# Kernel optimization log

Hardware: AMD Instinct MI355X
Metric: run time of the kernel (lower is better)

## Reference

```python
import jax, jax.numpy as jnp
import numpy as np

WINDOW_SIZE = 512
NUM_HEADS = 16
HIDDEN = 1024
HEAD_DIM = HIDDEN // NUM_HEADS
SCALING = HEAD_DIM ** (-0.5)


def sliding_window_mask(seq_len, window_size):
    # row i attends to cols j with i - w//2 <= j <= i + w//2 (clipped to bounds)
    i = jnp.arange(seq_len)[:, None]
    j = jnp.arange(seq_len)[None, :]
    half = window_size // 2
    return jnp.abs(i - j) <= half  # [S, S] bool


def setup_inputs() -> dict:
    key = jax.random.key(0)
    k0, k1, k2, k3, k4 = jax.random.split(key, 5)
    B, S = 2, 2048
    hidden_states = jax.random.normal(k0, (B, S, HIDDEN), dtype=jnp.float32)
    scale = 0.02
    Wq = jax.random.normal(k1, (HIDDEN, HIDDEN), dtype=jnp.float32) * scale
    Wk = jax.random.normal(k2, (HIDDEN, HIDDEN), dtype=jnp.float32) * scale
    Wv = jax.random.normal(k3, (HIDDEN, HIDDEN), dtype=jnp.float32) * scale
    Wo = jax.random.normal(k4, (HIDDEN, HIDDEN), dtype=jnp.float32) * scale
    return {"hidden_states": hidden_states, "Wq": Wq, "Wk": Wk, "Wv": Wv, "Wo": Wo}


def reference(hidden_states, Wq, Wk, Wv, Wo):
    B, S, _ = hidden_states.shape
    # nn.Linear(bias=False): y = x @ W.T
    def proj(x, W):
        y = jnp.einsum('bsh,oh->bso', x, W)
        return y.reshape(B, S, NUM_HEADS, HEAD_DIM).transpose(0, 2, 1, 3)  # [B,H,S,D]

    q = proj(hidden_states, Wq)
    k = proj(hidden_states, Wk)
    v = proj(hidden_states, Wv)

    mask = sliding_window_mask(S, WINDOW_SIZE)  # [S,S]
    scores = jnp.einsum('bhsd,bhtd->bhst', q, k) * SCALING  # [B,H,S,S]
    scores = jnp.where(mask[None, None], scores, -jnp.inf)
    attn = jax.nn.softmax(scores, axis=-1)
    out = jnp.einsum('bhst,bhtd->bhsd', attn, v)
    out = out.transpose(0, 2, 1, 3).reshape(B, S, HIDDEN)
    out = jnp.einsum('bsh,oh->bso', out, Wo)
    return out, attn
```

## Files before the change

### kernel.cpp

```cpp
#include <hip/hip_runtime.h>

typedef unsigned short u16;
typedef __attribute__((ext_vector_type(8))) __bf16 bf16x8;
typedef __attribute__((ext_vector_type(4))) float f32x4;

#define DEV __device__ __forceinline__
#define SEQ 2048
#define SWZ(r) ((((r) & 7)) ^ (((r) >> 3) & 7))

DEV void async16(void* lds, const void* gptr) {
  __builtin_amdgcn_global_load_lds(
      (const __attribute__((address_space(1))) unsigned int*)gptr,
      (__attribute__((address_space(3))) unsigned int*)lds, 16, 0, 0);
}

DEV u16 f2bf(float x) {
  unsigned u = __float_as_uint(x);
  return (u16)((u + 0x7fffu + ((u >> 16) & 1u)) >> 16);
}

DEV f32x4 mfma(bf16x8 a, bf16x8 b, f32x4 c) {
  return __builtin_amdgcn_mfma_f32_16x16x32_bf16(a, b, c, 0, 0, 0);
}

__global__ __launch_bounds__(256) void k_cvt_all(
    const float* __restrict__ hs, const float* __restrict__ wq,
    const float* __restrict__ wk, const float* __restrict__ wv,
    const float* __restrict__ wo, u16* __restrict__ X16,
    u16* __restrict__ W16) {
  int b = blockIdx.x;
  const float* src;
  u16* dst;
  int off;
  if (b < 4096) {
    src = hs;
    dst = X16;
    off = b * 1024;
  } else {
    int b2 = b - 4096;
    int w = b2 >> 10;
    src = (w == 0) ? wq : (w == 1) ? wk : (w == 2) ? wv : wo;
    dst = W16 + (size_t)w * 1048576;
    off = (b2 & 1023) * 1024;
  }
  int i = off + threadIdx.x * 4;
  float4 v = *(const float4*)(src + i);
  *(ushort4*)(dst + i) = make_ushort4(f2bf(v.x), f2bf(v.y), f2bf(v.z), f2bf(v.w));
}

DEV void gemm_mainloop(const u16* __restrict__ A, const u16* __restrict__ B,
                       int K, u16* As, u16* Bs, f32x4 (&acc)[4][4], int tid) {
  const int wid = tid >> 6, lane = tid & 63;
  const int wm = wid >> 1, wn = wid & 1;
  const int quad = lane >> 4, l15 = lane & 15;
  const int ci0 = tid, ci1 = tid + 256;
  const int r0 = ci0 >> 2, g0 = (ci0 & 3) ^ (r0 & 3);
  const int r1 = ci1 >> 2, g1 = (ci1 & 3) ^ (r1 & 3);
  u16* ldsA0 = As + wid * 512;
  u16* ldsA1 = As + wid * 512 + 2048;
  u16* ldsB0 = Bs + wid * 512;
  u16* ldsB1 = Bs + wid * 512 + 2048;

  for (int k0 = 0; k0 < K; k0 += 32) {
    __syncthreads();
    async16(ldsA0, A + (size_t)r0 * K + k0 + g0 * 8);
    async16(ldsA1, A + (size_t)r1 * K + k0 + g1 * 8);
    async16(ldsB0, B + (size_t)r0 * K + k0 + g0 * 8);
    async16(ldsB1, B + (size_t)r1 * K + k0 + g1 * 8);
    __syncthreads();
    bf16x8 af[4], bf[4];
#pragma unroll
    for (int mt = 0; mt < 4; ++mt) {
      int row = wm * 64 + mt * 16 + l15;
      af[mt] = *(const bf16x8*)(As + row * 32 + (quad ^ (row & 3)) * 8);
    }
#pragma unroll
    for (int nt = 0; nt < 4; ++nt) {
      int row = wn * 64 + nt * 16 + l15;
      bf[nt] = *(const bf16x8*)(Bs + row * 32 + (quad ^ (row & 3)) * 8);
    }
#pragma unroll
    for (int mt = 0; mt < 4; ++mt)
#pragma unroll
      for (int nt = 0; nt < 4; ++nt)
        acc[mt][nt] = mfma(af[mt], bf[nt], acc[mt][nt]);
  }
}

__global__ __launch_bounds__(256) void k_gemm_qkv(
    const u16* __restrict__ X, const u16* __restrict__ Wq,
    const u16* __restrict__ Wk, const u16* __restrict__ Wv,
    u16* __restrict__ Q16, u16* __restrict__ K16, u16* __restrict__ V16) {
  __shared__ u16 As[128 * 32], Bs[128 * 32];
  const int tid = threadIdx.x;
  const int bm = blockIdx.x, bn = blockIdx.y, z = blockIdx.z;
  const u16* B = (z == 0) ? Wq : (z == 1) ? Wk : Wv;
  u16* dst = (z == 0) ? Q16 : (z == 1) ? K16 : V16;
  const float sc = (z == 0) ? 0.125f : 1.0f;
  f32x4 acc[4][4];
#pragma unroll
  for (int i = 0; i < 4; ++i)
#pragma unroll
    for (int j = 0; j < 4; ++j) acc[i][j] = (f32x4){0.f, 0.f, 0.f, 0.f};
  gemm_mainloop(X + (size_t)bm * 128 * 1024, B + (size_t)bn * 128 * 1024, 1024,
                As, Bs, acc, tid);
  const int wid = tid >> 6, lane = tid & 63;
  const int wm = wid >> 1, wn = wid & 1, quad = lane >> 4, l15 = lane & 15;
#pragma unroll
  for (int mt = 0; mt < 4; ++mt)
#pragma unroll
    for (int nt = 0; nt < 4; ++nt)
#pragma unroll
      for (int r = 0; r < 4; ++r) {
        int row = bm * 128 + wm * 64 + mt * 16 + quad * 4 + r;
        int col = bn * 128 + wn * 64 + nt * 16 + l15;
        int b = row >> 11, s = row & 2047, h = col >> 6, d = col & 63;
        int bh = b * 16 + h;
        dst[((size_t)bh * SEQ + s) * 64 + d] = f2bf(acc[mt][nt][r] * sc);
      }
}

__global__ __launch_bounds__(256) void k_gemm_out(const u16* __restrict__ A,
                                                  const u16* __restrict__ Bw,
                                                  float* __restrict__ out) {
  __shared__ u16 As[64 * 32], Bs[128 * 32];
  const int tid = threadIdx.x;
  const int wid = tid >> 6, lane = tid & 63;
  const int wm = wid >> 1, wn = wid & 1;
  const int quad = lane >> 4, l15 = lane & 15;
  const int rA = tid >> 2, gA = (tid & 3) ^ (rA & 3);
  const int r1 = (tid + 256) >> 2, g1 = ((tid + 256) & 3) ^ (r1 & 3);
  const u16* Ab = A + (size_t)blockIdx.x * 64 * 1024;
  const u16* Bb = Bw + (size_t)blockIdx.y * 128 * 1024;
  f32x4 acc[2][4];
#pragma unroll
  for (int i = 0; i < 2; ++i)
#pragma unroll
    for (int j = 0; j < 4; ++j) acc[i][j] = (f32x4){0.f, 0.f, 0.f, 0.f};

  for (int k0 = 0; k0 < 1024; k0 += 32) {
    __syncthreads();
    async16(As + wid * 512, Ab + (size_t)rA * 1024 + k0 + gA * 8);
    async16(Bs + wid * 512, Bb + (size_t)rA * 1024 + k0 + gA * 8);
    async16(Bs + wid * 512 + 2048, Bb + (size_t)r1 * 1024 + k0 + g1 * 8);
    __syncthreads();
    bf16x8 af[2], bf[4];
#pragma unroll
    for (int mt = 0; mt < 2; ++mt) {
      int row = wm * 32 + mt * 16 + l15;
      af[mt] = *(const bf16x8*)(As + row * 32 + (quad ^ (row & 3)) * 8);
    }
#pragma unroll
    for (int nt = 0; nt < 4; ++nt) {
      int row = wn * 64 + nt * 16 + l15;
      bf[nt] = *(const bf16x8*)(Bs + row * 32 + (quad ^ (row & 3)) * 8);
    }
#pragma unroll
    for (int mt = 0; mt < 2; ++mt)
#pragma unroll
      for (int nt = 0; nt < 4; ++nt)
        acc[mt][nt] = mfma(af[mt], bf[nt], acc[mt][nt]);
  }
#pragma unroll
  for (int mt = 0; mt < 2; ++mt)
#pragma unroll
    for (int nt = 0; nt < 4; ++nt)
#pragma unroll
      for (int r = 0; r < 4; ++r) {
        int row = blockIdx.x * 64 + wm * 32 + mt * 16 + quad * 4 + r;
        int col = blockIdx.y * 128 + wn * 64 + nt * 16 + l15;
        out[(size_t)row * 1024 + col] = acc[mt][nt][r];
      }
}

__global__ __launch_bounds__(256, 2) void k_attn(
    const u16* __restrict__ Q16, const u16* __restrict__ K16,
    const u16* __restrict__ V16, float* __restrict__ attn_out,
    u16* __restrict__ O16) {
  __shared__ union alignas(16) U {
    struct {
      u16 Qt[4096];
      u16 Kt[3][4096];
      u16 Vt[3][4096];
      u16 P[2][64 * 72];
    } s;
    float Pf[2][64 * 68];
  } sm;
  __shared__ float rowsum[64];

  const int tid = threadIdx.x, wid = tid >> 6, lane = tid & 63;
  const int quad = lane >> 4, l15 = lane & 15;
  const int qbase = blockIdx.x * 64;
  const int bh = blockIdx.y;
  const int b = bh >> 4, h = bh & 15;
  const u16* Qb = Q16 + ((size_t)bh * SEQ + qbase) * 64;
  const u16* Kb = K16 + (size_t)bh * SEQ * 64;
  const u16* Vb = V16 + (size_t)bh * SEQ * 64;
  float* attn_b = attn_out + (size_t)bh * SEQ * SEQ;

  const int r0 = tid >> 3, g0 = (tid & 7) ^ SWZ(r0);
  const int r1 = r0 + 32, g1 = (tid & 7) ^ SWZ(r1);

  const int tlo = qbase >= 256 ? 0 : (256 - qbase) >> 6;
  const int thi_raw = (SEQ - 64 - qbase + 256) >> 6;
  const int thi = thi_raw > 8 ? 8 : thi_raw;

  auto stage = [&](int t) {
    int jb = qbase - 256 + t * 64;
    u16* Kd = sm.s.Kt[t % 3];
    u16* Vd = sm.s.Vt[t % 3];
    async16(Kd + wid * 512, Kb + (size_t)(jb + r0) * 64 + g0 * 8);
    async16(Kd + wid * 512 + 2048, Kb + (size_t)(jb + r1) * 64 + g1 * 8);
    async16(Vd + wid * 512, Vb + (size_t)(jb + r0) * 64 + g0 * 8);
    async16(Vd + wid * 512 + 2048, Vb + (size_t)(jb + r1) * 64 + g1 * 8);
  };

  async16(sm.s.Qt + wid * 512, Qb + r0 * 64 + g0 * 8);
  async16(sm.s.Qt + wid * 512 + 2048, Qb + (size_t)r1 * 64 + g1 * 8);
  stage(tlo);
  if (tlo + 1 <= thi) stage(tlo + 1);
  if (tid < 64) rowsum[tid] = 0.f;

  float racc[4][4];
  f32x4 oacc[4];
#pragma unroll
  for (int mt = 0; mt < 4; ++mt) {
    oacc[mt] = (f32x4){0.f, 0.f, 0.f, 0.f};
#pragma unroll
    for (int r = 0; r < 4; ++r) racc[mt][r] = 0.f;
  }
  unsigned stash[9][8];
  bf16x8 bv_prev[2];
  bf16x8 aq[4][2];
  bool aq_loaded = false;
  const int d = wid * 16 + l15;

#pragma unroll
  for (int t = 0; t < 9; ++t) {
    if (t < tlo || t > thi) continue;
    const int jbase = qbase - 256 + t * 64;
    if (t + 1 <= thi)
      asm volatile("s_waitcnt vmcnt(4) lgkmcnt(0)" ::: "memory");
    else
      asm volatile("s_waitcnt vmcnt(0) lgkmcnt(0)" ::: "memory");
    __builtin_amdgcn_s_barrier();
    if (t + 2 <= thi) stage(t + 2);
    if (!aq_loaded) {
      aq_loaded = true;
#pragma unroll
      for (int mt = 0; mt < 4; ++mt)
#pragma unroll
        for (int ks = 0; ks < 2; ++ks) {
          int row = mt * 16 + l15;
          aq[mt][ks] = *(const bf16x8*)(sm.s.Qt + row * 64 +
                                        (((ks * 4 + quad) ^ SWZ(row)) * 8));
        }
    }
    if (t > tlo) {
      const u16* Pp = sm.s.P[(t + 1) & 1];
#pragma unroll
      for (int mt = 0; mt < 4; ++mt) {
        int row = mt * 16 + l15;
        bf16x8 ap0 = *(const bf16x8*)(Pp + row * 72 + quad * 8);
        bf16x8 ap1 = *(const bf16x8*)(Pp + row * 72 + 32 + quad * 8);
        oacc[mt] = mfma(ap0, bv_prev[0], oacc[mt]);
        oacc[mt] = mfma(ap1, bv_prev[1], oacc[mt]);
      }
    }
    const u16* Kt = sm.s.Kt[t % 3];
    const u16* Vtp = sm.s.Vt[t % 3];
    bf16x8 bq[2];
#pragma unroll
    for (int ks = 0; ks < 2; ++ks) {
      int row = wid * 16 + l15;
      bq[ks] = *(const bf16x8*)(Kt + row * 64 + (((ks * 4 + quad) ^ SWZ(row)) * 8));
    }
#pragma unroll
    for (int ks = 0; ks < 2; ++ks)
#pragma unroll
      for (int jj = 0; jj < 8; ++jj) {
        int j = ks * 32 + quad * 8 + jj;
        int slot = (d >> 3) ^ SWZ(j);
        bv_prev[ks][jj] = *(const __bf16*)(Vtp + j * 64 + slot * 8 + (d & 7));
      }
    u16* Pc = sm.s.P[t & 1];
    const int jcol = jbase + wid * 16 + l15;
#pragma unroll
    for (int mt = 0; mt < 4; ++mt) {
      f32x4 c = (f32x4){0.f, 0.f, 0.f, 0.f};
      c = mfma(aq[mt][0], bq[0], c);
      c = mfma(aq[mt][1], bq[1], c);
      unsigned p0 = 0, p1 = 0;
#pragma unroll
      for (int r = 0; r < 4; ++r) {
        int i_ = qbase + mt * 16 + quad * 4 + r;
        int dlt = i_ - jcol;
        dlt = dlt < 0 ? -dlt : dlt;
        float e = 0.f;
        if (dlt <= 256) e = __expf(c[r]);
        racc[mt][r] += e;
        unsigned eb = f2bf(e);
        Pc[(mt * 16 + quad * 4 + r) * 72 + wid * 16 + l15] = (u16)eb;
        if (r == 0) p0 = eb;
        if (r == 1) p0 |= eb << 16;
        if (r == 2) p1 = eb;
        if (r == 3) p1 |= eb << 16;
      }
      stash[t][mt * 2] = p0;
      stash[t][mt * 2 + 1] = p1;
    }
  }
  __syncthreads();
  {
    const u16* Pp = sm.s.P[thi & 1];
#pragma unroll
    for (int mt = 0; mt < 4; ++mt) {
      int row = mt * 16 + l15;
      bf16x8 ap0 = *(const bf16x8*)(Pp + row * 72 + quad * 8);
      bf16x8 ap1 = *(const bf16x8*)(Pp + row * 72 + 32 + quad * 8);
      oacc[mt] = mfma(ap0, bv_prev[0], oacc[mt]);
      oacc[mt] = mfma(ap1, bv_prev[1], oacc[mt]);
    }
  }

#pragma unroll
  for (int mt = 0; mt < 4; ++mt)
#pragma unroll
    for (int r = 0; r < 4; ++r) {
      float v = racc[mt][r];
      v += __shfl_xor(v, 1, 16);
      v += __shfl_xor(v, 2, 16);
      v += __shfl_xor(v, 4, 16);
      v += __shfl_xor(v, 8, 16);
      racc[mt][r] = v;
    }
  if (l15 == 0) {
#pragma unroll
    for (int mt = 0; mt < 4; ++mt)
#pragma unroll
      for (int r = 0; r < 4; ++r)
        atomicAdd(&rowsum[mt * 16 + quad * 4 + r], racc[mt][r]);
  }
  __syncthreads();
  float linv[4][4];
#pragma unroll
  for (int mt = 0; mt < 4; ++mt)
#pragma unroll
    for (int r = 0; r < 4; ++r)
      linv[mt][r] = 1.0f / rowsum[mt * 16 + quad * 4 + r];

#pragma unroll
  for (int mt = 0; mt < 4; ++mt)
#pragma unroll
    for (int r = 0; r < 4; ++r) {
      int i_ = qbase + mt * 16 + quad * 4 + r;
      O16[((size_t)b * SEQ + i_) * 1024 + h * 64 + d] =
          f2bf(oacc[mt][r] * linv[mt][r]);
    }

  const int wcol = (tid & 15) * 4, wrow = tid >> 4;
#pragma unroll
  for (int t = 0; t < 9; ++t) {
    if (t < tlo || t > thi) continue;
    const int jbase = qbase - 256 + t * 64;
    float* Pf = sm.Pf[t & 1];
#pragma unroll
    for (int mt = 0; mt < 4; ++mt) {
      unsigned p0 = stash[t][mt * 2], p1 = stash[t][mt * 2 + 1];
      int rb = mt * 16 + quad * 4;
      int cc = wid * 16 + l15;
      Pf[(rb + 0) * 68 + cc] = __uint_as_float(p0 << 16) * linv[mt][0];
      Pf[(rb + 1) * 68 + cc] = __uint_as_float(p0 & 0xffff0000u) * linv[mt][1];
      Pf[(rb + 2) * 68 + cc] = __uint_as_float(p1 << 16) * linv[mt][2];
      Pf[(rb + 3) * 68 + cc] = __uint_as_float(p1 & 0xffff0000u) * linv[mt][3];
    }
    asm volatile("s_waitcnt lgkmcnt(0)\n\ts_barrier" ::: "memory");
#pragma unroll
    for (int k = 0; k < 4; ++k) {
      int row = wrow + k * 16;
      f32x4 v = *(const f32x4*)(Pf + row * 68 + wcol);
      __builtin_nontemporal_store(
          v, (f32x4*)(attn_b + (size_t)(qbase + row) * SEQ + jbase + wcol));
    }
  }
}

extern "C" void kernel_launch(void* const* d_in, const int* in_sizes, int n_in,
                              void* d_out, int out_size, void* d_ws,
                              size_t ws_size, hipStream_t stream) {
  const float* hs = (const float*)d_in[0];
  const float* Wq = (const float*)d_in[1];
  const float* Wk = (const float*)d_in[2];
  const float* Wv = (const float*)d_in[3];
  const float* Wo = (const float*)d_in[4];
  float* out = (float*)d_out;
  float* attn = out + (size_t)4194304;

  u16* X16 = (u16*)d_ws;
  u16* Wq16 = X16 + 4194304;
  u16* Wk16 = Wq16 + 1048576;
  u16* Wv16 = Wk16 + 1048576;
  u16* Wo16 = Wv16 + 1048576;
  u16* Q16 = Wo16 + 1048576;
  u16* K16 = Q16 + 4194304;
  u16* V16 = K16 + 4194304;
  u16* O16 = V16 + 4194304;

  k_cvt_all<<<8192, 256, 0, stream>>>(hs, Wq, Wk, Wv, Wo, X16, Wq16);
  k_gemm_qkv<<<dim3(32, 8, 3), 256, 0, stream>>>(X16, Wq16, Wk16, Wv16, Q16,
                                                 K16, V16);
  k_attn<<<dim3(32, 32), 256, 0, stream>>>(Q16, K16, V16, attn, O16);
  k_gemm_out<<<dim3(64, 8), 256, 0, stream>>>(O16, Wo16, out);
}
```

Before: 579.9 us.

## Halve attention query tile to 32 rows and double-buffer K/V tiles

The attention kernel now handles 32 query rows per block instead of 64, which doubles the grid and raises the occupancy hint from 2 to 3 blocks per CU. Key/value tiles are now aligned to 64-column boundaries derived from the window range. The K/V ring drops from three buffers to two, with a plain block barrier replacing the explicit vmcnt-counted waits. This shrinks LDS and register use to fit more blocks per CU, at the cost of reloading each K/V tile for twice as many blocks and losing the deeper prefetch.

```diff
diff --git a/kernel.cpp b/kernel.cpp
--- a/kernel.cpp
+++ b/kernel.cpp
@@ -173,24 +173,24 @@
       }
 }
 
-__global__ __launch_bounds__(256, 2) void k_attn(
+__global__ __launch_bounds__(256, 3) void k_attn(
     const u16* __restrict__ Q16, const u16* __restrict__ K16,
     const u16* __restrict__ V16, float* __restrict__ attn_out,
     u16* __restrict__ O16) {
   __shared__ union alignas(16) U {
     struct {
-      u16 Qt[4096];
-      u16 Kt[3][4096];
-      u16 Vt[3][4096];
-      u16 P[2][64 * 72];
+      u16 Qt[2048];
+      u16 Kt[2][4096];
+      u16 Vt[2][4096];
+      u16 P[2][32 * 72];
     } s;
-    float Pf[2][64 * 68];
+    float Pf[2][32 * 68];
   } sm;
-  __shared__ float rowsum[64];
+  __shared__ float rowsum[32];
 
   const int tid = threadIdx.x, wid = tid >> 6, lane = tid & 63;
   const int quad = lane >> 4, l15 = lane & 15;
-  const int qbase = blockIdx.x * 64;
+  const int qbase = blockIdx.x * 32;
   const int bh = blockIdx.y;
   const int b = bh >> 4, h = bh & 15;
   const u16* Qb = Q16 + ((size_t)bh * SEQ + qbase) * 64;
@@ -201,54 +201,49 @@
   const int r0 = tid >> 3, g0 = (tid & 7) ^ SWZ(r0);
   const int r1 = r0 + 32, g1 = (tid & 7) ^ SWZ(r1);
 
-  const int tlo = qbase >= 256 ? 0 : (256 - qbase) >> 6;
-  const int thi_raw = (SEQ - 64 - qbase + 256) >> 6;
-  const int thi = thi_raw > 8 ? 8 : thi_raw;
+  const int u_lo = (qbase >= 256) ? ((qbase - 256) >> 6) : 0;
+  const int u_hi_raw = (qbase + 287) >> 6;
+  const int u_hi = u_hi_raw > 31 ? 31 : u_hi_raw;
+  const int nt = u_hi - u_lo + 1;
 
   auto stage = [&](int t) {
-    int jb = qbase - 256 + t * 64;
-    u16* Kd = sm.s.Kt[t % 3];
-    u16* Vd = sm.s.Vt[t % 3];
+    int jb = (u_lo + t) * 64;
+    u16* Kd = sm.s.Kt[t & 1];
+    u16* Vd = sm.s.Vt[t & 1];
     async16(Kd + wid * 512, Kb + (size_t)(jb + r0) * 64 + g0 * 8);
     async16(Kd + wid * 512 + 2048, Kb + (size_t)(jb + r1) * 64 + g1 * 8);
     async16(Vd + wid * 512, Vb + (size_t)(jb + r0) * 64 + g0 * 8);
     async16(Vd + wid * 512 + 2048, Vb + (size_t)(jb + r1) * 64 + g1 * 8);
   };
 
-  async16(sm.s.Qt + wid * 512, Qb + r0 * 64 + g0 * 8);
-  async16(sm.s.Qt + wid * 512 + 2048, Qb + (size_t)r1 * 64 + g1 * 8);
-  stage(tlo);
-  if (tlo + 1 <= thi) stage(tlo + 1);
-  if (tid < 64) rowsum[tid] = 0.f;
-
-  float racc[4][4];
-  f32x4 oacc[4];
-#pragma unroll
-  for (int mt = 0; mt < 4; ++mt) {
+  async16(sm.s.Qt + wid * 512, Qb + (size_t)r0 * 64 + g0 * 8);
+  stage(0);
+  if (tid < 32) rowsum[tid] = 0.f;
+
+  float racc[2][4];
+  f32x4 oacc[2];
+#pragma unroll
+  for (int mt = 0; mt < 2; ++mt) {
     oacc[mt] = (f32x4){0.f, 0.f, 0.f, 0.f};
 #pragma unroll
     for (int r = 0; r < 4; ++r) racc[mt][r] = 0.f;
   }
-  unsigned stash[9][8];
+  unsigned stash[9][4];
   bf16x8 bv_prev[2];
-  bf16x8 aq[4][2];
+  bf16x8 aq[2][2];
   bool aq_loaded = false;
   const int d = wid * 16 + l15;
 
 #pragma unroll
   for (int t = 0; t < 9; ++t) {
-    if (t < tlo || t > thi) continue;
-    const int jbase = qbase - 256 + t * 64;
-    if (t + 1 <= thi)
-      asm volatile("s_waitcnt vmcnt(4) lgkmcnt(0)" ::: "memory");
-    else
-      asm volatile("s_waitcnt vmcnt(0) lgkmcnt(0)" ::: "memory");
-    __builtin_amdgcn_s_barrier();
-    if (t + 2 <= thi) stage(t + 2);
+    if (t >= nt) continue;
+    const int jbase = (u_lo + t) * 64;
+    __syncthreads();
+    if (t + 1 < nt) stage(t + 1);
     if (!aq_loaded) {
       aq_loaded = true;
 #pragma unroll
-      for (int mt = 0; mt < 4; ++mt)
+      for (int mt = 0; mt < 2; ++mt)
 #pragma unroll
         for (int ks = 0; ks < 2; ++ks) {
           int row = mt * 16 + l15;
@@ -256,10 +251,10 @@
                                         (((ks * 4 + quad) ^ SWZ(row)) * 8));
         }
     }
-    if (t > tlo) {
+    if (t > 0) {
       const u16* Pp = sm.s.P[(t + 1) & 1];
 #pragma unroll
-      for (int mt = 0; mt < 4; ++mt) {
+      for (int mt = 0; mt < 2; ++mt) {
         int row = mt * 16 + l15;
         bf16x8 ap0 = *(const bf16x8*)(Pp + row * 72 + quad * 8);
         bf16x8 ap1 = *(const bf16x8*)(Pp + row * 72 + 32 + quad * 8);
@@ -267,8 +262,8 @@
         oacc[mt] = mfma(ap1, bv_prev[1], oacc[mt]);
       }
     }
-    const u16* Kt = sm.s.Kt[t % 3];
-    const u16* Vtp = sm.s.Vt[t % 3];
+    const u16* Kt = sm.s.Kt[t & 1];
+    const u16* Vtp = sm.s.Vt[t & 1];
     bf16x8 bq[2];
 #pragma unroll
     for (int ks = 0; ks < 2; ++ks) {
@@ -286,7 +281,7 @@
     u16* Pc = sm.s.P[t & 1];
     const int jcol = jbase + wid * 16 + l15;
 #pragma unroll
-    for (int mt = 0; mt < 4; ++mt) {
+    for (int mt = 0; mt < 2; ++mt) {
       f32x4 c = (f32x4){0.f, 0.f, 0.f, 0.f};
       c = mfma(aq[mt][0], bq[0], c);
       c = mfma(aq[mt][1], bq[1], c);
@@ -312,9 +307,9 @@
   }
   __syncthreads();
   {
-    const u16* Pp = sm.s.P[thi & 1];
-#pragma unroll
-    for (int mt = 0; mt < 4; ++mt) {
+    const u16* Pp = sm.s.P[(nt + 1) & 1];
+#pragma unroll
+    for (int mt = 0; mt < 2; ++mt) {
       int row = mt * 16 + l15;
       bf16x8 ap0 = *(const bf16x8*)(Pp + row * 72 + quad * 8);
       bf16x8 ap1 = *(const bf16x8*)(Pp + row * 72 + 32 + quad * 8);
@@ -324,7 +319,7 @@
   }
 
 #pragma unroll
-  for (int mt = 0; mt < 4; ++mt)
+  for (int mt = 0; mt < 2; ++mt)
 #pragma unroll
     for (int r = 0; r < 4; ++r) {
       float v = racc[mt][r];
@@ -336,21 +331,21 @@
     }
   if (l15 == 0) {
 #pragma unroll
-    for (int mt = 0; mt < 4; ++mt)
+    for (int mt = 0; mt < 2; ++mt)
 #pragma unroll
       for (int r = 0; r < 4; ++r)
         atomicAdd(&rowsum[mt * 16 + quad * 4 + r], racc[mt][r]);
   }
   __syncthreads();
-  float linv[4][4];
-#pragma unroll
-  for (int mt = 0; mt < 4; ++mt)
+  float linv[2][4];
+#pragma unroll
+  for (int mt = 0; mt < 2; ++mt)
 #pragma unroll
     for (int r = 0; r < 4; ++r)
       linv[mt][r] = 1.0f / rowsum[mt * 16 + quad * 4 + r];
 
 #pragma unroll
-  for (int mt = 0; mt < 4; ++mt)
+  for (int mt = 0; mt < 2; ++mt)
 #pragma unroll
     for (int r = 0; r < 4; ++r) {
       int i_ = qbase + mt * 16 + quad * 4 + r;
@@ -361,11 +356,11 @@
   const int wcol = (tid & 15) * 4, wrow = tid >> 4;
 #pragma unroll
   for (int t = 0; t < 9; ++t) {
-    if (t < tlo || t > thi) continue;
-    const int jbase = qbase - 256 + t * 64;
+    if (t >= nt) continue;
+    const int jbase = (u_lo + t) * 64;
     float* Pf = sm.Pf[t & 1];
 #pragma unroll
-    for (int mt = 0; mt < 4; ++mt) {
+    for (int mt = 0; mt < 2; ++mt) {
       unsigned p0 = stash[t][mt * 2], p1 = stash[t][mt * 2 + 1];
       int rb = mt * 16 + quad * 4;
       int cc = wid * 16 + l15;
@@ -376,7 +371,7 @@
     }
     asm volatile("s_waitcnt lgkmcnt(0)\n\ts_barrier" ::: "memory");
 #pragma unroll
-    for (int k = 0; k < 4; ++k) {
+    for (int k = 0; k < 2; ++k) {
       int row = wrow + k * 16;
       f32x4 v = *(const f32x4*)(Pf + row * 68 + wcol);
       __builtin_nontemporal_store(
@@ -409,6 +404,6 @@
   k_cvt_all<<<8192, 256, 0, stream>>>(hs, Wq, Wk, Wv, Wo, X16, Wq16);
   k_gemm_qkv<<<dim3(32, 8, 3), 256, 0, stream>>>(X16, Wq16, Wk16, Wv16, Q16,
                                                  K16, V16);
-  k_attn<<<dim3(32, 32), 256, 0, stream>>>(Q16, K16, V16, attn, O16);
+  k_attn<<<dim3(64, 32), 256, 0, stream>>>(Q16, K16, V16, attn, O16);
   k_gemm_out<<<dim3(64, 8), 256, 0, stream>>>(O16, Wo16, out);
 }
```

After: 574.6 us. About the same (-0.9%).
